# Performance work log

Measured on AMD Instinct MI355X. Metric: run time of the kernel, lower is better.

Reference implementation:

```python
import jax, jax.numpy as jnp
import numpy as np


def setup_inputs() -> dict:
    key = jax.random.key(0)
    k1, k2, k3 = jax.random.split(key, 3)
    B, L, D = 4, 2056, 1024  # L = K + T = 8 + 2048
    x = jax.random.normal(k1, (B, L, D), dtype=jnp.float32)
    # Linear weights stored as (in_features, out_features); no bias (config.bias=False)
    W_attn = jax.random.normal(k2, (D, 3 * D), dtype=jnp.float32) * 0.02
    W_proj = jax.random.normal(k3, (D, D), dtype=jnp.float32) * 0.02
    return {"x": x, "W_attn": W_attn, "W_proj": W_proj, "n_head": 16, "n_memory": 8}


def reference(x, W_attn, W_proj, n_head, n_memory):
    B, L, C = x.shape
    K = n_memory
    T = L - K
    hd = C // n_head
    scale = 1.0 / np.sqrt(hd).astype(np.float32)

    qkv = x @ W_attn                      # (B, L, 3C)
    q, k, v = jnp.split(qkv, 3, axis=2)
    # (B, H, L, hd)
    q = q.reshape(B, L, n_head, hd).transpose(0, 2, 1, 3)
    k = k.reshape(B, L, n_head, hd).transpose(0, 2, 1, 3)
    v = v.reshape(B, L, n_head, hd).transpose(0, 2, 1, 3)

    att = jnp.einsum("bhqd,bhkd->bhqk", q, k) * scale  # (B, H, L, L)

    # Mask: all-True except the (seq x seq) block which is causal (lower-tri).
    # Memory rows (first K) attend everywhere; seq rows attend to all memory + causal seq.
    mask = jnp.ones((L, L), dtype=bool)
    seq_causal = jnp.tril(jnp.ones((T, T), dtype=bool))
    mask = mask.at[K:, K:].set(seq_causal)

    att = jnp.where(mask[None, None, :, :], att, jnp.float32(-jnp.inf))
    att = jax.nn.softmax(att, axis=-1)

    y = jnp.einsum("bhqk,bhkd->bhqd", att, v)  # (B, H, L, hd)
    y = y.transpose(0, 2, 1, 3).reshape(B, L, C)
    return y @ W_proj
```

## Files before the change

### kernel.cpp

```cpp
#include <hip/hip_runtime.h>
#include <hip/hip_bf16.h>
#include <hip/hip_fp16.h>

typedef _Float16 f16x8 __attribute__((ext_vector_type(8)));
typedef _Float16 f16x4 __attribute__((ext_vector_type(4)));
typedef float f32x4 __attribute__((ext_vector_type(4)));

typedef const __attribute__((address_space(1))) void gvoid_t;
typedef __attribute__((address_space(3))) void svoid_t;

constexpr int Bb = 4, Lq = 2056, Dd = 1024, NH = 16, HD = 64, NMEM = 8;
constexpr int Mtot = Bb * Lq;
constexpr int KEYS = 64;
constexpr int NT = (Lq + KEYS - 1) / KEYS;
constexpr int NTQP = 17;
constexpr int LqV = 2064;

__device__ inline float fexp2(float x) {
  float r;
  asm("v_exp_f32 %0, %1" : "=v"(r) : "v"(x));
  return r;
}

__global__ __launch_bounds__(256) void cast_f16(const float* __restrict__ in,
                                                _Float16* __restrict__ out, int n8) {
  int i = blockIdx.x * blockDim.x + threadIdx.x;
  if (i >= n8) return;
  const float4* p = reinterpret_cast<const float4*>(in) + (size_t)i * 2;
  float4 a = p[0], b = p[1];
  f16x8 o;
  o[0] = (_Float16)a.x; o[1] = (_Float16)a.y; o[2] = (_Float16)a.z; o[3] = (_Float16)a.w;
  o[4] = (_Float16)b.x; o[5] = (_Float16)b.y; o[6] = (_Float16)b.z; o[7] = (_Float16)b.w;
  *(reinterpret_cast<f16x8*>(out) + i) = o;
}

__global__ void transpose_cast(const float* __restrict__ in, _Float16* __restrict__ out,
                               int rows, int cols) {
  __shared__ float t[32][33];
  int c0 = blockIdx.x * 32, r0 = blockIdx.y * 32;
  int tx = threadIdx.x, ty = threadIdx.y;
#pragma unroll
  for (int i = 0; i < 4; ++i)
    t[ty + i * 8][tx] = in[(size_t)(r0 + ty + i * 8) * cols + c0 + tx];
  __syncthreads();
#pragma unroll
  for (int i = 0; i < 4; ++i)
    out[(size_t)(c0 + ty + i * 8) * rows + r0 + tx] = (_Float16)t[tx][ty + i * 8];
}

template <int EPI>
__global__ __launch_bounds__(256) void gemm_f16(
    const _Float16* __restrict__ A, const _Float16* __restrict__ Bt,
    int M, int N, int Kd, float* __restrict__ Cf,
    _Float16* __restrict__ qout, _Float16* __restrict__ kout, _Float16* __restrict__ vtout) {
  constexpr int BM = 128, BN = 128, BK = 64;
  __shared__ _Float16 smem[2][2 * BM * BK];
  const int tid = threadIdx.x;
  const int wid = tid >> 6, lane = tid & 63;
  const int wr = wid >> 1, wc = wid & 1;
  const int l16 = lane & 15, lq = lane >> 4;

  const int gx = gridDim.x;
  const int nwg = gx * gridDim.y;
  const int i0 = blockIdx.y * gx + blockIdx.x;
  const int cpx = nwg >> 3;
  const int logical = (i0 & 7) * cpx + (i0 >> 3);
  const int m0 = (logical / gx) * BM, n0 = (logical % gx) * BN;

  f32x4 acc[4][4];
#pragma unroll
  for (int i = 0; i < 4; ++i)
#pragma unroll
    for (int j = 0; j < 4; ++j) acc[i][j] = (f32x4){0.f, 0.f, 0.f, 0.f};

  auto stage = [&](int sb, int kt) {
    const size_t kbase = (size_t)kt * BK;
    _Float16* sm = smem[sb];
#pragma unroll
    for (int c = 0; c < 4; ++c) {
      int q = wid * 256 + c * 64 + lane;
      int r = q >> 3, cc = q & 7;
      int gr = m0 + r; gr = gr < M ? gr : M - 1;
      const _Float16* src = A + (size_t)gr * Kd + kbase + ((cc ^ (r & 7)) << 3);
      __builtin_amdgcn_global_load_lds((gvoid_t*)src,
          (svoid_t*)(sm + (size_t)(wid * 256 + c * 64) * 8), 16, 0, 0);
    }
#pragma unroll
    for (int c = 0; c < 4; ++c) {
      int q = wid * 256 + c * 64 + lane;
      int r = q >> 3, cc = q & 7;
      const _Float16* src = Bt + (size_t)(n0 + r) * Kd + kbase + ((cc ^ (r & 7)) << 3);
      __builtin_amdgcn_global_load_lds((gvoid_t*)src,
          (svoid_t*)(sm + BM * BK + (size_t)(wid * 256 + c * 64) * 8), 16, 0, 0);
    }
  };

  const int KT = Kd / BK;
  stage(0, 0);
  __syncthreads();
  int sbuf = 0;
  for (int kt = 0; kt < KT; ++kt) {
    if (kt + 1 < KT) stage(sbuf ^ 1, kt + 1);
    const _Float16* sm = smem[sbuf];
#pragma unroll
    for (int kk = 0; kk < 2; ++kk) {
      f16x8 af[4], bfr[4];
#pragma unroll
      for (int i = 0; i < 4; ++i) {
        int r = wr * 64 + i * 16 + l16;
        int off = r * 64 + (((kk * 4 + lq) ^ (r & 7)) << 3);
        af[i] = *(const f16x8*)(sm + off);
      }
#pragma unroll
      for (int j = 0; j < 4; ++j) {
        int r = wc * 64 + j * 16 + l16;
        int off = BM * BK + r * 64 + (((kk * 4 + lq) ^ (r & 7)) << 3);
        bfr[j] = *(const f16x8*)(sm + off);
      }
#pragma unroll
      for (int i = 0; i < 4; ++i)
#pragma unroll
        for (int j = 0; j < 4; ++j)
          acc[i][j] = __builtin_amdgcn_mfma_f32_16x16x32_f16(af[i], bfr[j], acc[i][j], 0, 0, 0);
    }
    __syncthreads();
    sbuf ^= 1;
  }

  if (EPI == 1 && n0 >= 2 * Dd) {
#pragma unroll
    for (int i = 0; i < 4; ++i) {
      int mb = m0 + wr * 64 + i * 16 + lq * 4;
      if (mb >= M) continue;
      int b = mb / Lq, l = mb - b * Lq;
#pragma unroll
      for (int j = 0; j < 4; ++j) {
        int n = n0 + wc * 64 + j * 16 + l16;
        int h = (n >> 6) & 15, d = n & 63;
        if (l + 4 <= Lq) {
          int kk = l & 63;
          int ks = kk >> 5, rem = kk & 31, half = rem >> 4, idx = rem & 15;
          int col = (l & ~63) + (ks * 4 + (idx >> 2)) * 8 + half * 4;
          f16x4 pk;
          pk[0] = (_Float16)acc[i][j][0]; pk[1] = (_Float16)acc[i][j][1];
          pk[2] = (_Float16)acc[i][j][2]; pk[3] = (_Float16)acc[i][j][3];
          *(f16x4*)(vtout + ((size_t)(b * NH + h) * HD + d) * LqV + col) = pk;
        } else {
#pragma unroll
          for (int r = 0; r < 4; ++r) {
            int m = mb + r;
            if (m >= M) continue;
            int b2 = m / Lq, l2 = m - b2 * Lq;
            int kk = l2 & 63;
            int ks = kk >> 5, rem = kk & 31, half = rem >> 4, idx = rem & 15;
            int col = (l2 & ~63) + (ks * 4 + (idx >> 2)) * 8 + half * 4 + (idx & 3);
            vtout[((size_t)(b2 * NH + h) * HD + d) * LqV + col] = (_Float16)acc[i][j][r];
          }
        }
      }
    }
  } else {
#pragma unroll
    for (int i = 0; i < 4; ++i) {
#pragma unroll
      for (int r = 0; r < 4; ++r) {
        int m = m0 + wr * 64 + i * 16 + lq * 4 + r;
        if (m >= M) continue;
        if (EPI == 0) {
#pragma unroll
          for (int j = 0; j < 4; ++j) {
            int n = n0 + wc * 64 + j * 16 + l16;
            Cf[(size_t)m * N + n] = acc[i][j][r];
          }
        } else {
          int b = m / Lq, l = m - b * Lq;
#pragma unroll
          for (int j = 0; j < 4; ++j) {
            int n = n0 + wc * 64 + j * 16 + l16;
            int which = n >> 10, h = (n >> 6) & 15, d = n & 63;
            int bh = b * NH + h;
            _Float16 v = (_Float16)acc[i][j][r];
            if (which == 0)
              qout[((size_t)bh * Lq + l) * HD + d] = v;
            else
              kout[((size_t)bh * Lq + l) * HD + d] = v;
          }
        }
      }
    }
  }
}

__global__ __launch_bounds__(256) void attn_f16(const _Float16* __restrict__ qm,
                                                const _Float16* __restrict__ km,
                                                const _Float16* __restrict__ vt,
                                                _Float16* __restrict__ y) {
  __shared__ _Float16 kls[2][KEYS * HD];
  __shared__ _Float16 vls[2][KEYS * HD];

  const int i0 = blockIdx.y * (int)gridDim.x + blockIdx.x;
  const int logical = (i0 & 7) * (NTQP * Bb * NH / 8) + (i0 >> 3);
  const int bh = logical / NTQP;
  const int px = logical % NTQP;

  const int wid = threadIdx.x >> 6, lane = threadIdx.x & 63;
  const int l16 = lane & 15, lq = lane >> 4;

  const _Float16* qbase = qm + (size_t)bh * Lq * HD;
  const _Float16* kbase = km + (size_t)bh * Lq * HD;
  const _Float16* vbase = vt + (size_t)bh * HD * LqV;
  const int b = bh >> 4, h = bh & 15;

  const _Float16 QSC = (_Float16)(0.125f * 1.44269504f);

  f16x8 ones;
#pragma unroll
  for (int e = 0; e < 8; ++e) ones[e] = (_Float16)1.0f;

  const int qA = (wid * 2 + 0) * 64 + lane, qB = (wid * 2 + 1) * 64 + lane;
  const int rA = qA >> 3, cA = qA & 7;
  const int rB = qB >> 3, cB = qB & 7;
  const int ofA = (cA ^ (rA & 7)) << 3;
  const int ofB = (cB ^ (rB & 7)) << 3;
  _Float16* dKA0 = &kls[0][(wid * 2 + 0) * 512]; _Float16* dKB0 = &kls[0][(wid * 2 + 1) * 512];
  _Float16* dKA1 = &kls[1][(wid * 2 + 0) * 512]; _Float16* dKB1 = &kls[1][(wid * 2 + 1) * 512];
  _Float16* dVA0 = &vls[0][(wid * 2 + 0) * 512]; _Float16* dVB0 = &vls[0][(wid * 2 + 1) * 512];
  _Float16* dVA1 = &vls[1][(wid * 2 + 0) * 512]; _Float16* dVB1 = &vls[1][(wid * 2 + 1) * 512];

  const int nseg = (px == 0) ? 1 : 2;
  for (int seg = 0; seg < nseg; ++seg) {
    const int qt = (px == 0) ? 0 : (seg == 0 ? NT - px : px);
    const int qr0 = qt * 64 + wid * 16;

    int qrow = qr0 + l16; if (qrow > Lq - 1) qrow = Lq - 1;
    f16x8 qf0 = *(const f16x8*)(qbase + (size_t)qrow * HD + lq * 8);
    f16x8 qf1 = *(const f16x8*)(qbase + (size_t)qrow * HD + 32 + lq * 8);
#pragma unroll
    for (int e = 0; e < 8; ++e) {
      qf0[e] *= QSC;
      qf1[e] *= QSC;
    }

    const int irow = qr0 + l16;
    const int kmax = (irow < NMEM) ? (Lq - 1) : (irow < Lq - 1 ? irow : Lq - 1);

    f32x4 o[4];
#pragma unroll
    for (int dt = 0; dt < 4; ++dt) o[dt] = (f32x4){0.f, 0.f, 0.f, 0.f};
    f32x4 ol = (f32x4){0.f, 0.f, 0.f, 0.f};

    const int ntiles = (qt == 0) ? NT : (qt + 1 < NT ? qt + 1 : NT);

    const _Float16* pkA = kbase + (size_t)rA * HD + ofA;
    const _Float16* pkB = kbase + (size_t)rB * HD + ofB;
    const _Float16* pvA = vbase + (size_t)rA * LqV + ofA;
    const _Float16* pvB = vbase + (size_t)rB * LqV + ofB;

    auto stage_fast = [&](_Float16* dK0, _Float16* dK1, _Float16* dV0, _Float16* dV1) {
      __builtin_amdgcn_global_load_lds((gvoid_t*)pkA, (svoid_t*)dK0, 16, 0, 0);
      __builtin_amdgcn_global_load_lds((gvoid_t*)pkB, (svoid_t*)dK1, 16, 0, 0);
      __builtin_amdgcn_global_load_lds((gvoid_t*)pvA, (svoid_t*)dV0, 16, 0, 0);
      __builtin_amdgcn_global_load_lds((gvoid_t*)pvB, (svoid_t*)dV1, 16, 0, 0);
      pkA += KEYS * HD; pkB += KEYS * HD; pvA += KEYS; pvB += KEYS;
    };
    auto stage_clamp = [&](_Float16* dK0, _Float16* dK1, _Float16* dV0, _Float16* dV1) {
      int keyA = 2048 + rA; if (keyA > Lq - 1) keyA = Lq - 1;
      int keyB = 2048 + rB; if (keyB > Lq - 1) keyB = Lq - 1;
      __builtin_amdgcn_global_load_lds((gvoid_t*)(kbase + (size_t)keyA * HD + ofA),
                                       (svoid_t*)dK0, 16, 0, 0);
      __builtin_amdgcn_global_load_lds((gvoid_t*)(kbase + (size_t)keyB * HD + ofB),
                                       (svoid_t*)dK1, 16, 0, 0);
      int kcA = 2048 + ofA; if (kcA + 8 > LqV) kcA = LqV - 8;
      int kcB = 2048 + ofB; if (kcB + 8 > LqV) kcB = LqV - 8;
      __builtin_amdgcn_global_load_lds((gvoid_t*)(vbase + (size_t)rA * LqV + kcA),
                                       (svoid_t*)dV0, 16, 0, 0);
      __builtin_amdgcn_global_load_lds((gvoid_t*)(vbase + (size_t)rB * LqV + kcB),
                                       (svoid_t*)dV1, 16, 0, 0);
    };

    auto compute = [&](const _Float16* Kl, const _Float16* Vl, int t) {
      const bool fastw = ((t + 1) * KEYS <= qr0);
      const int lim = kmax - t * KEYS;
#pragma unroll
      for (int ks = 0; ks < 2; ++ks) {
        const int r0 = ks * 32 + l16, r1 = r0 + 16;
        f16x8 ka0 = *(const f16x8*)(Kl + r0 * 64 + ((lq ^ (r0 & 7)) << 3));
        f16x8 kb0 = *(const f16x8*)(Kl + r0 * 64 + (((4 + lq) ^ (r0 & 7)) << 3));
        f16x8 ka1 = *(const f16x8*)(Kl + r1 * 64 + ((lq ^ (r1 & 7)) << 3));
        f16x8 kb1 = *(const f16x8*)(Kl + r1 * 64 + (((4 + lq) ^ (r1 & 7)) << 3));
        f32x4 s0 = (f32x4){0.f, 0.f, 0.f, 0.f};
        f32x4 s1 = (f32x4){0.f, 0.f, 0.f, 0.f};
        __builtin_amdgcn_s_setprio(1);
        s0 = __builtin_amdgcn_mfma_f32_16x16x32_f16(ka0, qf0, s0, 0, 0, 0);
        s0 = __builtin_amdgcn_mfma_f32_16x16x32_f16(kb0, qf1, s0, 0, 0, 0);
        s1 = __builtin_amdgcn_mfma_f32_16x16x32_f16(ka1, qf0, s1, 0, 0, 0);
        s1 = __builtin_amdgcn_mfma_f32_16x16x32_f16(kb1, qf1, s1, 0, 0, 0);
        __builtin_amdgcn_s_setprio(0);

        f16x8 pf;
        if (fastw) {
#pragma unroll
          for (int r = 0; r < 4; ++r) {
            pf[r] = (_Float16)fexp2(s0[r]);
            pf[4 + r] = (_Float16)fexp2(s1[r]);
          }
        } else {
          const int kb = ks * 32 + lq * 4;
#pragma unroll
          for (int r = 0; r < 4; ++r) {
            pf[r] = (kb + r <= lim) ? (_Float16)fexp2(s0[r]) : (_Float16)0.f;
            pf[4 + r] = (kb + 16 + r <= lim) ? (_Float16)fexp2(s1[r]) : (_Float16)0.f;
          }
        }

        __builtin_amdgcn_s_setprio(1);
        ol = __builtin_amdgcn_mfma_f32_16x16x32_f16(pf, ones, ol, 0, 0, 0);
#pragma unroll
        for (int dt = 0; dt < 4; ++dt) {
          const int vr = dt * 16 + l16;
          const int g = ks * 4 + lq;
          f16x8 vf = *(const f16x8*)(Vl + vr * 64 + ((g ^ (vr & 7)) << 3));
          o[dt] = __builtin_amdgcn_mfma_f32_16x16x32_f16(pf, vf, o[dt], 0, 0, 0);
        }
        __builtin_amdgcn_s_setprio(0);
      }
    };

    stage_fast(dKA0, dKB0, dVA0, dVB0);
    __syncthreads();
    int t = 0;
    for (;;) {
      {
        int nxt = t + 1;
        if (nxt < ntiles) {
          if (nxt == NT - 1) stage_clamp(dKA1, dKB1, dVA1, dVB1);
          else stage_fast(dKA1, dKB1, dVA1, dVB1);
        }
      }
      compute(kls[0], vls[0], t);
      __syncthreads();
      if (++t >= ntiles) break;
      {
        int nxt = t + 1;
        if (nxt < ntiles) {
          if (nxt == NT - 1) stage_clamp(dKA0, dKB0, dVA0, dVB0);
          else stage_fast(dKA0, dKB0, dVA0, dVB0);
        }
      }
      compute(kls[1], vls[1], t);
      __syncthreads();
      if (++t >= ntiles) break;
    }

#pragma unroll
    for (int r = 0; r < 4; ++r) {
      int orow = qr0 + lq * 4 + r;
      if (orow >= Lq) continue;
      float inv = 1.0f / ol[r];
#pragma unroll
      for (int dt = 0; dt < 4; ++dt)
        y[((size_t)(b * Lq + orow)) * Dd + h * HD + dt * 16 + l16] = (_Float16)(o[dt][r] * inv);
    }
  }
}

extern "C" void kernel_launch(void* const* d_in, const int* in_sizes, int n_in,
                              void* d_out, int out_size, void* d_ws, size_t ws_size,
                              hipStream_t stream) {
  (void)in_sizes; (void)n_in; (void)out_size; (void)ws_size;
  const float* x = (const float*)d_in[0];
  const float* W_attn = (const float*)d_in[1];
  const float* W_proj = (const float*)d_in[2];
  float* out = (float*)d_out;

  char* w = (char*)d_ws;
  _Float16* xh  = (_Float16*)(w);
  _Float16* wta = (_Float16*)(w + 16842752);
  _Float16* wtp = (_Float16*)(w + 23134208);
  _Float16* qh  = (_Float16*)(w + 25231360);
  _Float16* kh  = (_Float16*)(w + 42074112);
  _Float16* vth = (_Float16*)(w + 58916864);
  _Float16* yh  = xh;

  cast_f16<<<dim3((Mtot * Dd) / 8 / 256), dim3(256), 0, stream>>>(x, xh, (Mtot * Dd) / 8);
  transpose_cast<<<dim3(3 * Dd / 32, Dd / 32), dim3(32, 8), 0, stream>>>(W_attn, wta, Dd, 3 * Dd);
  transpose_cast<<<dim3(Dd / 32, Dd / 32), dim3(32, 8), 0, stream>>>(W_proj, wtp, Dd, Dd);

  gemm_f16<1><<<dim3(3 * Dd / 128, (Mtot + 127) / 128), dim3(256), 0, stream>>>(
      xh, wta, Mtot, 3 * Dd, Dd, nullptr, qh, kh, vth);

  attn_f16<<<dim3(NTQP, Bb * NH), dim3(256), 0, stream>>>(qh, kh, vth, yh);

  gemm_f16<0><<<dim3(Dd / 128, (Mtot + 127) / 128), dim3(256), 0, stream>>>(
      yh, wtp, Mtot, Dd, Dd, out, nullptr, nullptr, nullptr);
}
```

Before: 204.0 us.

## Double attention key tile to 128 keys per pipeline stage

Measured after the change: 220.1 us. 1.08x slower.

```diff
diff --git a/kernel.cpp b/kernel.cpp
--- a/kernel.cpp
+++ b/kernel.cpp
@@ -11,7 +11,7 @@
 
 constexpr int Bb = 4, Lq = 2056, Dd = 1024, NH = 16, HD = 64, NMEM = 8;
 constexpr int Mtot = Bb * Lq;
-constexpr int KEYS = 64;
+constexpr int KEYS = 128;
 constexpr int NT = (Lq + KEYS - 1) / KEYS;
 constexpr int NTQP = 17;
 constexpr int LqV = 2064;
@@ -217,19 +217,30 @@
 #pragma unroll
   for (int e = 0; e < 8; ++e) ones[e] = (_Float16)1.0f;
 
-  const int qA = (wid * 2 + 0) * 64 + lane, qB = (wid * 2 + 1) * 64 + lane;
-  const int rA = qA >> 3, cA = qA & 7;
-  const int rB = qB >> 3, cB = qB & 7;
-  const int ofA = (cA ^ (rA & 7)) << 3;
-  const int ofB = (cB ^ (rB & 7)) << 3;
-  _Float16* dKA0 = &kls[0][(wid * 2 + 0) * 512]; _Float16* dKB0 = &kls[0][(wid * 2 + 1) * 512];
-  _Float16* dKA1 = &kls[1][(wid * 2 + 0) * 512]; _Float16* dKB1 = &kls[1][(wid * 2 + 1) * 512];
-  _Float16* dVA0 = &vls[0][(wid * 2 + 0) * 512]; _Float16* dVB0 = &vls[0][(wid * 2 + 1) * 512];
-  _Float16* dVA1 = &vls[1][(wid * 2 + 0) * 512]; _Float16* dVB1 = &vls[1][(wid * 2 + 1) * 512];
+  int rK[4], oK[4];
+  int rV[4], oV[4];
+#pragma unroll
+  for (int c = 0; c < 4; ++c) {
+    int q = (wid * 4 + c) * 64 + lane;
+    rK[c] = q >> 3;
+    oK[c] = (((q & 7) ^ (rK[c] & 7)) << 3);
+    rV[c] = q >> 4;
+    int cc = q & 15, blk = cc >> 3, c8 = cc & 7;
+    oV[c] = blk * 64 + ((c8 ^ (rV[c] & 7)) << 3);
+  }
+  _Float16* dK[2][4];
+  _Float16* dV[2][4];
+#pragma unroll
+  for (int bf = 0; bf < 2; ++bf)
+#pragma unroll
+    for (int c = 0; c < 4; ++c) {
+      dK[bf][c] = &kls[bf][(size_t)(wid * 4 + c) * 512];
+      dV[bf][c] = &vls[bf][(size_t)(wid * 4 + c) * 512];
+    }
 
   const int nseg = (px == 0) ? 1 : 2;
   for (int seg = 0; seg < nseg; ++seg) {
-    const int qt = (px == 0) ? 0 : (seg == 0 ? NT - px : px);
+    const int qt = (px == 0) ? 0 : (seg == 0 ? 33 - px : px);
     const int qr0 = qt * 64 + wid * 16;
 
     int qrow = qr0 + l16; if (qrow > Lq - 1) qrow = Lq - 1;
@@ -249,40 +260,47 @@
     for (int dt = 0; dt < 4; ++dt) o[dt] = (f32x4){0.f, 0.f, 0.f, 0.f};
     f32x4 ol = (f32x4){0.f, 0.f, 0.f, 0.f};
 
-    const int ntiles = (qt == 0) ? NT : (qt + 1 < NT ? qt + 1 : NT);
-
-    const _Float16* pkA = kbase + (size_t)rA * HD + ofA;
-    const _Float16* pkB = kbase + (size_t)rB * HD + ofB;
-    const _Float16* pvA = vbase + (size_t)rA * LqV + ofA;
-    const _Float16* pvB = vbase + (size_t)rB * LqV + ofB;
-
-    auto stage_fast = [&](_Float16* dK0, _Float16* dK1, _Float16* dV0, _Float16* dV1) {
-      __builtin_amdgcn_global_load_lds((gvoid_t*)pkA, (svoid_t*)dK0, 16, 0, 0);
-      __builtin_amdgcn_global_load_lds((gvoid_t*)pkB, (svoid_t*)dK1, 16, 0, 0);
-      __builtin_amdgcn_global_load_lds((gvoid_t*)pvA, (svoid_t*)dV0, 16, 0, 0);
-      __builtin_amdgcn_global_load_lds((gvoid_t*)pvB, (svoid_t*)dV1, 16, 0, 0);
-      pkA += KEYS * HD; pkB += KEYS * HD; pvA += KEYS; pvB += KEYS;
+    const int need = (qt + 2) >> 1;
+    const int ntiles = (qt == 0) ? NT : (need < NT ? need : NT);
+
+    const _Float16* pk[4];
+    const _Float16* pv[4];
+#pragma unroll
+    for (int c = 0; c < 4; ++c) {
+      pk[c] = kbase + (size_t)rK[c] * HD + oK[c];
+      pv[c] = vbase + (size_t)rV[c] * LqV + oV[c];
+    }
+
+    auto stage_fast = [&](int bf) {
+#pragma unroll
+      for (int c = 0; c < 4; ++c)
+        __builtin_amdgcn_global_load_lds((gvoid_t*)pk[c], (svoid_t*)dK[bf][c], 16, 0, 0);
+#pragma unroll
+      for (int c = 0; c < 4; ++c)
+        __builtin_amdgcn_global_load_lds((gvoid_t*)pv[c], (svoid_t*)dV[bf][c], 16, 0, 0);
+#pragma unroll
+      for (int c = 0; c < 4; ++c) { pk[c] += KEYS * HD; pv[c] += KEYS; }
     };
-    auto stage_clamp = [&](_Float16* dK0, _Float16* dK1, _Float16* dV0, _Float16* dV1) {
-      int keyA = 2048 + rA; if (keyA > Lq - 1) keyA = Lq - 1;
-      int keyB = 2048 + rB; if (keyB > Lq - 1) keyB = Lq - 1;
-      __builtin_amdgcn_global_load_lds((gvoid_t*)(kbase + (size_t)keyA * HD + ofA),
-                                       (svoid_t*)dK0, 16, 0, 0);
-      __builtin_amdgcn_global_load_lds((gvoid_t*)(kbase + (size_t)keyB * HD + ofB),
-                                       (svoid_t*)dK1, 16, 0, 0);
-      int kcA = 2048 + ofA; if (kcA + 8 > LqV) kcA = LqV - 8;
-      int kcB = 2048 + ofB; if (kcB + 8 > LqV) kcB = LqV - 8;
-      __builtin_amdgcn_global_load_lds((gvoid_t*)(vbase + (size_t)rA * LqV + kcA),
-                                       (svoid_t*)dV0, 16, 0, 0);
-      __builtin_amdgcn_global_load_lds((gvoid_t*)(vbase + (size_t)rB * LqV + kcB),
-                                       (svoid_t*)dV1, 16, 0, 0);
+    auto stage_clamp = [&](int bf) {
+#pragma unroll
+      for (int c = 0; c < 4; ++c) {
+        int key = 2048 + rK[c]; if (key > Lq - 1) key = Lq - 1;
+        __builtin_amdgcn_global_load_lds((gvoid_t*)(kbase + (size_t)key * HD + oK[c]),
+                                         (svoid_t*)dK[bf][c], 16, 0, 0);
+      }
+#pragma unroll
+      for (int c = 0; c < 4; ++c) {
+        int kc = 2048 + oV[c]; if (kc + 8 > LqV) kc = LqV - 8;
+        __builtin_amdgcn_global_load_lds((gvoid_t*)(vbase + (size_t)rV[c] * LqV + kc),
+                                         (svoid_t*)dV[bf][c], 16, 0, 0);
+      }
     };
 
     auto compute = [&](const _Float16* Kl, const _Float16* Vl, int t) {
       const bool fastw = ((t + 1) * KEYS <= qr0);
       const int lim = kmax - t * KEYS;
 #pragma unroll
-      for (int ks = 0; ks < 2; ++ks) {
+      for (int ks = 0; ks < 4; ++ks) {
         const int r0 = ks * 32 + l16, r1 = r0 + 16;
         f16x8 ka0 = *(const f16x8*)(Kl + r0 * 64 + ((lq ^ (r0 & 7)) << 3));
         f16x8 kb0 = *(const f16x8*)(Kl + r0 * 64 + (((4 + lq) ^ (r0 & 7)) << 3));
@@ -318,23 +336,23 @@
 #pragma unroll
         for (int dt = 0; dt < 4; ++dt) {
           const int vr = dt * 16 + l16;
-          const int g = ks * 4 + lq;
-          f16x8 vf = *(const f16x8*)(Vl + vr * 64 + ((g ^ (vr & 7)) << 3));
+          const int g = (ks & 1) * 4 + lq;
+          f16x8 vf = *(const f16x8*)(Vl + vr * KEYS + (ks >> 1) * 64 + ((g ^ (vr & 7)) << 3));
           o[dt] = __builtin_amdgcn_mfma_f32_16x16x32_f16(pf, vf, o[dt], 0, 0, 0);
         }
         __builtin_amdgcn_s_setprio(0);
       }
     };
 
-    stage_fast(dKA0, dKB0, dVA0, dVB0);
+    stage_fast(0);
     __syncthreads();
     int t = 0;
     for (;;) {
       {
         int nxt = t + 1;
         if (nxt < ntiles) {
-          if (nxt == NT - 1) stage_clamp(dKA1, dKB1, dVA1, dVB1);
-          else stage_fast(dKA1, dKB1, dVA1, dVB1);
+          if (nxt == NT - 1) stage_clamp(1);
+          else stage_fast(1);
         }
       }
       compute(kls[0], vls[0], t);
@@ -343,8 +361,8 @@
       {
         int nxt = t + 1;
         if (nxt < ntiles) {
-          if (nxt == NT - 1) stage_clamp(dKA0, dKB0, dVA0, dVB0);
-          else stage_fast(dKA0, dKB0, dVA0, dVB0);
+          if (nxt == NT - 1) stage_clamp(0);
+          else stage_fast(0);
         }
       }
       compute(kls[1], vls[1], t);
```
